# Kernel tuning notes

Hardware: AMD Instinct MI355X
Metric: run time of the kernel (lower is better)

Reference implementation:

```python
import jax, jax.numpy as jnp
import numpy as np

ATOM_FDIM = 35
BOND_FDIM = 5
MAX_NB = 10
HIDDEN = 128
DEPTH = 6
N_ATOMS = 100000
N_BONDS = 220000
N_MESS = 20000
N_MOLS = 2000


def setup_inputs() -> dict:
    key = jax.random.key(0)
    ks = jax.random.split(key, 10)
    fatoms = jax.random.uniform(ks[0], (N_ATOMS, ATOM_FDIM), dtype=jnp.float32)
    fbonds = jax.random.uniform(ks[1], (N_BONDS, ATOM_FDIM + BOND_FDIM), dtype=jnp.float32)
    tree_message = jax.random.normal(ks[2], (N_MESS, HIDDEN), dtype=jnp.float32)
    tree_message = tree_message.at[0].set(0.0)  # index 0 is the zero-padding message
    agraph = jax.random.randint(ks[3], (N_ATOMS, MAX_NB), 0, N_MESS + N_BONDS, dtype=jnp.int32)
    bgraph = jax.random.randint(ks[4], (N_BONDS, MAX_NB), 0, N_MESS + N_BONDS, dtype=jnp.int32)
    mol_ids = jnp.sort(jax.random.randint(ks[5], (N_ATOMS,), 0, N_MOLS, dtype=jnp.int32))
    # learned parameters (torch Linear stores W as [out, in]; we keep [in, out])
    def lin(k, fan_in, fan_out):
        bound = 1.0 / np.sqrt(fan_in)
        return jax.random.uniform(k, (fan_in, fan_out), minval=-bound, maxval=bound, dtype=jnp.float32)
    W_i = lin(ks[6], ATOM_FDIM + BOND_FDIM, HIDDEN)
    W_h = lin(ks[7], HIDDEN, HIDDEN)
    W_o = lin(ks[8], ATOM_FDIM + HIDDEN, HIDDEN)
    b_o = jax.random.uniform(ks[9], (HIDDEN,), minval=-1.0 / np.sqrt(ATOM_FDIM + HIDDEN), maxval=1.0 / np.sqrt(ATOM_FDIM + HIDDEN), dtype=jnp.float32)
    return {
        'fatoms': fatoms, 'fbonds': fbonds, 'tree_message': tree_message,
        'agraph': agraph, 'bgraph': bgraph, 'mol_ids': mol_ids, 'n_mols': N_MOLS,
        'W_i': W_i, 'W_h': W_h, 'W_o': W_o, 'b_o': b_o,
    }


def reference(fatoms, fbonds, tree_message, agraph, bgraph, mol_ids, n_mols, W_i, W_h, W_o, b_o):
    binput = fbonds @ W_i                    # [B, H]
    graph_message = jax.nn.relu(binput)
    for _ in range(DEPTH - 1):
        message = jnp.concatenate([tree_message, graph_message], axis=0)  # [M+B, H]
        nei = message[bgraph].sum(axis=1)    # gather [B, MAX_NB, H] -> sum -> [B, H]
        graph_message = jax.nn.relu(binput + nei @ W_h)
    message = jnp.concatenate([tree_message, graph_message], axis=0)
    nei_a = message[agraph].sum(axis=1)      # [A, H]
    ainput = jnp.concatenate([fatoms, nei_a], axis=1)  # [A, ATOM_FDIM+H]
    atom_hiddens = jax.nn.relu(ainput @ W_o + b_o)     # [A, H]
    # mean-pool per molecule (scope)
    sums = jax.ops.segment_sum(atom_hiddens, mol_ids, num_segments=n_mols)
    counts = jax.ops.segment_sum(jnp.ones((atom_hiddens.shape[0],), dtype=atom_hiddens.dtype), mol_ids, num_segments=n_mols)
    mol_vecs = sums / jnp.maximum(counts, 1.0)[:, None]
    return mol_vecs
```

## Files before the change

### kernel.cpp

```cpp
#include <hip/hip_runtime.h>

#define N_ATOMS   100000
#define N_BONDS   220000
#define N_MESS    20000
#define N_MSG     (N_MESS + N_BONDS)
#define ATOM_FDIM 35
#define BOND_FDIM 5
#define BOND_IN   (ATOM_FDIM + BOND_FDIM)
#define H         128
#define MAX_NB    10
#define DEPTH     6
#define KO        (ATOM_FDIM + H)
#define KC        192

typedef __attribute__((ext_vector_type(8))) short short8;
typedef __attribute__((ext_vector_type(4))) float f32x4;

static __device__ __forceinline__ unsigned short f2bf(float f) {
    union { float f; unsigned int i; } v; v.f = f;
    unsigned int x = v.i;
    return (unsigned short)((x + 0x7FFFu + ((x >> 16) & 1u)) >> 16);
}

static __device__ __forceinline__ float ub2f(unsigned int v, int b) {
    return (float)((v >> (b * 8)) & 0xffu);
}

static __device__ __forceinline__ unsigned char q8(float x) {
    int q = __float2int_rn(x);
    q = q < 0 ? 0 : (q > 255 ? 255 : q);
    return (unsigned char)q;
}

#define PTa (N_BONDS * BOND_IN)
#define PTb (PTa + H * KC)
#define PTc (PTb + H * KC)

__global__ __launch_bounds__(256) void prep(
    const float* __restrict__ fbonds,
    const float* __restrict__ Wi, const float* __restrict__ Wh,
    const float* __restrict__ Wo,
    ushort* __restrict__ fbc, ushort* __restrict__ WT,
    ushort* __restrict__ WoT, float* __restrict__ out, int n_out)
{
    int i = blockIdx.x * 256 + threadIdx.x;
    if (i < PTa) {
        fbc[i] = f2bf(fbonds[i]);
    } else if (i < PTb) {
        int j = i - PTa;
        int n = j / KC, k = j - n * KC;
        float v = (k < BOND_IN) ? Wi[k * H + n]
                : (k < BOND_IN + H) ? Wh[(k - BOND_IN) * H + n] : 0.f;
        WT[j] = f2bf(v);
    } else if (i < PTc) {
        int j = i - PTb;
        int n = j / KC, k = j - n * KC;
        float v = (k < H) ? Wo[(ATOM_FDIM + k) * H + n]
                : (k < KO) ? Wo[(k - H) * H + n] : 0.f;
        WoT[j] = f2bf(v);
    } else {
        int j = i - PTc;
        if (j < n_out) out[j] = 0.f;
    }
}

__global__ __launch_bounds__(256) void qtree(
    const float* __restrict__ tree,
    unsigned char* __restrict__ qA, unsigned char* __restrict__ qB,
    float2* __restrict__ sA, float2* __restrict__ sB)
{
    int row = blockIdx.x * 4 + (threadIdx.x >> 6);
    int lane = threadIdx.x & 63;
    float2 v = *(const float2*)&tree[(size_t)row * H + lane * 2];
    float mx = fmaxf(v.x, v.y), mn = fminf(v.x, v.y);
    #pragma unroll
    for (int d = 1; d <= 32; d <<= 1) {
        mx = fmaxf(mx, __shfl_xor(mx, d));
        mn = fminf(mn, __shfl_xor(mn, d));
    }
    float rng = mx - mn;
    float inv = (rng > 0.f) ? 255.f / rng : 0.f;
    int q0 = q8((v.x - mn) * inv);
    int q1 = q8((v.y - mn) * inv);
    unsigned short pk = (unsigned short)(q0 | (q1 << 8));
    ((unsigned short*)qA)[(size_t)row * 64 + lane] = pk;
    ((unsigned short*)qB)[(size_t)row * 64 + lane] = pk;
    if (lane == 0) {
        float2 s = make_float2(rng * (1.f / 255.f), mn);
        sA[row] = s; sB[row] = s;
    }
}

static __device__ __forceinline__ uint4 gather8(
    const unsigned char* __restrict__ msgq, const float2* __restrict__ scl,
    const int* __restrict__ gidx, int c16)
{
    int idx[MAX_NB];
    #pragma unroll
    for (int n = 0; n < MAX_NB; n++) idx[n] = gidx[n];
    float2 so[MAX_NB];
    uint2 d[MAX_NB];
    #pragma unroll
    for (int n = 0; n < MAX_NB; n++) {
        so[n] = scl[idx[n]];
        d[n] = *(const uint2*)(msgq + (size_t)idx[n] * H + c16 * 8);
    }
    float s0=0.f,s1=0.f,s2=0.f,s3=0.f,s4=0.f,s5=0.f,s6=0.f,s7=0.f;
    float off = 0.f;
    #pragma unroll
    for (int n = 0; n < MAX_NB; n++) {
        float sc = so[n].x; off += so[n].y;
        s0 += sc * ub2f(d[n].x, 0); s1 += sc * ub2f(d[n].x, 1);
        s2 += sc * ub2f(d[n].x, 2); s3 += sc * ub2f(d[n].x, 3);
        s4 += sc * ub2f(d[n].y, 0); s5 += sc * ub2f(d[n].y, 1);
        s6 += sc * ub2f(d[n].y, 2); s7 += sc * ub2f(d[n].y, 3);
    }
    s0 += off; s1 += off; s2 += off; s3 += off;
    s4 += off; s5 += off; s6 += off; s7 += off;
    uint4 pk;
    pk.x = ((unsigned)f2bf(s1) << 16) | (unsigned)f2bf(s0);
    pk.y = ((unsigned)f2bf(s3) << 16) | (unsigned)f2bf(s2);
    pk.z = ((unsigned)f2bf(s5) << 16) | (unsigned)f2bf(s4);
    pk.w = ((unsigned)f2bf(s7) << 16) | (unsigned)f2bf(s6);
    return pk;
}

static __device__ __forceinline__ void quant_epilogue(
    f32x4 c00, f32x4 c01, f32x4 c10, f32x4 c11,
    int tid, int row_base,
    float* rmx, float* qp,
    unsigned char* __restrict__ gq, float2* __restrict__ scout)
{
    int lane = tid & 63, wv = tid >> 6;
    int m_lane = lane & 15, quad = lane >> 4;
    int n0 = wv * 32;

    float v00[4], v01[4], v10[4], v11[4];
    #pragma unroll
    for (int r = 0; r < 4; r++) {
        v00[r] = fmaxf(c00[r], 0.f); v01[r] = fmaxf(c01[r], 0.f);
        v10[r] = fmaxf(c10[r], 0.f); v11[r] = fmaxf(c11[r], 0.f);
    }
    #pragma unroll
    for (int r = 0; r < 4; r++) {
        float mx0 = fmaxf(v00[r], v01[r]);
        float mx1 = fmaxf(v10[r], v11[r]);
        #pragma unroll
        for (int d = 1; d <= 8; d <<= 1) {
            mx0 = fmaxf(mx0, __shfl_xor(mx0, d));
            mx1 = fmaxf(mx1, __shfl_xor(mx1, d));
        }
        if (m_lane == 0) {
            rmx[(quad * 4 + r) * 4 + wv]      = mx0;
            rmx[(quad * 4 + r + 16) * 4 + wv] = mx1;
        }
    }
    __syncthreads();
    if (tid < 32) {
        float mx = fmaxf(fmaxf(rmx[tid * 4], rmx[tid * 4 + 1]),
                         fmaxf(rmx[tid * 4 + 2], rmx[tid * 4 + 3]));
        qp[tid] = (mx > 0.f) ? 255.f / mx : 0.f;
        scout[row_base + tid] = make_float2(mx * (1.f / 255.f), 0.f);
    }
    __syncthreads();
    #pragma unroll
    for (int r = 0; r < 4; r++) {
        int r0 = quad * 4 + r, r1 = r0 + 16;
        float i0 = qp[r0], i1 = qp[r1];
        gq[(size_t)(row_base + r0) * H + n0 + m_lane]      = q8(v00[r] * i0);
        gq[(size_t)(row_base + r0) * H + n0 + 16 + m_lane] = q8(v01[r] * i0);
        gq[(size_t)(row_base + r1) * H + n0 + m_lane]      = q8(v10[r] * i1);
        gq[(size_t)(row_base + r1) * H + n0 + 16 + m_lane] = q8(v11[r] * i1);
    }
}

__global__ __launch_bounds__(256, 4) void binput0(
    const ushort* __restrict__ fbc, const ushort* __restrict__ WT,
    unsigned char* __restrict__ gq_out, float2* __restrict__ sc_out)
{
    __shared__ ushort Xlds[32 * 25 * 8];
    __shared__ float rmx[32 * 4];
    __shared__ float qp[32];

    int tid = threadIdx.x;
    int bond0 = blockIdx.x * 32;
    int lane = tid & 63, wv = tid >> 6;

    if (tid < 160) {
        int b = tid / 5, k8 = tid - b * 5;
        *(short8*)&Xlds[(b * 25 + k8) * 8] =
            *(const short8*)&fbc[(size_t)bond0 * BOND_IN + tid * 8];
    }
    if (tid < 96) {
        int b = tid / 3, k8 = 5 + (tid - b * 3);
        *(float4*)&Xlds[(b * 25 + k8) * 8] = float4{0.f, 0.f, 0.f, 0.f};
    }
    __syncthreads();

    int n0 = wv * 32;
    int m_lane = lane & 15, quad = lane >> 4;
    f32x4 c00 = {0,0,0,0}, c01 = {0,0,0,0}, c10 = {0,0,0,0}, c11 = {0,0,0,0};

    #pragma unroll
    for (int s = 0; s < 2; s++) {
        short8 a0 = *(const short8*)&Xlds[((m_lane)      * 25 + s * 4 + quad) * 8];
        short8 a1 = *(const short8*)&Xlds[((16 + m_lane) * 25 + s * 4 + quad) * 8];
        short8 b0 = *(const short8*)&WT[(size_t)(n0 + m_lane)      * KC + s * 32 + quad * 8];
        short8 b1 = *(const short8*)&WT[(size_t)(n0 + 16 + m_lane) * KC + s * 32 + quad * 8];
        c00 = __builtin_amdgcn_mfma_f32_16x16x32_bf16(a0, b0, c00, 0, 0, 0);
        c01 = __builtin_amdgcn_mfma_f32_16x16x32_bf16(a0, b1, c01, 0, 0, 0);
        c10 = __builtin_amdgcn_mfma_f32_16x16x32_bf16(a1, b0, c10, 0, 0, 0);
        c11 = __builtin_amdgcn_mfma_f32_16x16x32_bf16(a1, b1, c11, 0, 0, 0);
    }

    quant_epilogue(c00, c01, c10, c11, tid, bond0, rmx, qp, gq_out, sc_out);
}

__global__ __launch_bounds__(256, 4) void mp_round(
    const unsigned char* __restrict__ msg_in, const float2* __restrict__ sc_in,
    const ushort* __restrict__ fbc, const int* __restrict__ bgraph,
    const ushort* __restrict__ WT,
    unsigned char* __restrict__ gq_out, float2* __restrict__ sc_out)
{
    __shared__ ushort Xlds[32 * 25 * 8];
    __shared__ float rmx[32 * 4];
    __shared__ float qp[32];

    int tid = threadIdx.x;
    int bond0 = blockIdx.x * 32;
    int lane = tid & 63, wv = tid >> 6;
    int q = lane >> 4, c16 = lane & 15;

    if (tid < 160) {
        int b = tid / 5, k8 = tid - b * 5;
        *(short8*)&Xlds[(b * 25 + k8) * 8] =
            *(const short8*)&fbc[(size_t)bond0 * BOND_IN + tid * 8];
    }
    if (tid < 96) {
        int b = tid / 3, k8 = 21 + (tid - b * 3);
        *(float4*)&Xlds[(b * 25 + k8) * 8] = float4{0.f, 0.f, 0.f, 0.f};
    }
    #pragma unroll
    for (int g = 0; g < 2; g++) {
        int b = wv + 4 * (g * 4 + q);
        uint4 pk = gather8(msg_in, sc_in, bgraph + (size_t)(bond0 + b) * MAX_NB, c16);
        *(uint4*)&Xlds[(b * 25 + 5 + c16) * 8] = pk;
    }
    __syncthreads();

    int n0 = wv * 32;
    int m_lane = lane & 15, quad = lane >> 4;
    f32x4 c00 = {0,0,0,0}, c01 = {0,0,0,0}, c10 = {0,0,0,0}, c11 = {0,0,0,0};

    #pragma unroll
    for (int s = 0; s < KC / 32; s++) {
        short8 a0 = *(const short8*)&Xlds[((m_lane)      * 25 + s * 4 + quad) * 8];
        short8 a1 = *(const short8*)&Xlds[((16 + m_lane) * 25 + s * 4 + quad) * 8];
        short8 b0 = *(const short8*)&WT[(size_t)(n0 + m_lane)      * KC + s * 32 + quad * 8];
        short8 b1 = *(const short8*)&WT[(size_t)(n0 + 16 + m_lane) * KC + s * 32 + quad * 8];
        c00 = __builtin_amdgcn_mfma_f32_16x16x32_bf16(a0, b0, c00, 0, 0, 0);
        c01 = __builtin_amdgcn_mfma_f32_16x16x32_bf16(a0, b1, c01, 0, 0, 0);
        c10 = __builtin_amdgcn_mfma_f32_16x16x32_bf16(a1, b0, c10, 0, 0, 0);
        c11 = __builtin_amdgcn_mfma_f32_16x16x32_bf16(a1, b1, c11, 0, 0, 0);
    }

    quant_epilogue(c00, c01, c10, c11, tid, bond0, rmx, qp, gq_out, sc_out);
}

__global__ __launch_bounds__(256, 4) void atom_mfma(
    const float* __restrict__ fatoms, const unsigned char* __restrict__ msg,
    const float2* __restrict__ scl,
    const int* __restrict__ agraph, const ushort* __restrict__ WoT,
    const float* __restrict__ bo, const int* __restrict__ mol_ids,
    float* __restrict__ out)
{
    __shared__ ushort Xlds[32 * 25 * 8];
    __shared__ float htile[32 * H];
    __shared__ int mlds[32];

    int tid = threadIdx.x;
    int a0 = blockIdx.x * 32;
    int lane = tid & 63, wv = tid >> 6;
    int q = lane >> 4, c16 = lane & 15;

    for (int i = tid; i < 32 * ATOM_FDIM; i += 256) {
        int b = i / ATOM_FDIM, t = i - b * ATOM_FDIM;
        int k = H + t;
        Xlds[(b * 25 + (k >> 3)) * 8 + (k & 7)] = f2bf(fatoms[(size_t)a0 * ATOM_FDIM + i]);
    }
    if (tid < 160) {
        int b = tid / 5, k = 163 + (tid - b * 5);
        Xlds[(b * 25 + (k >> 3)) * 8 + (k & 7)] = 0;
    }
    if (tid < 96) {
        int b = tid / 3, k8 = 21 + (tid - b * 3);
        *(float4*)&Xlds[(b * 25 + k8) * 8] = float4{0.f, 0.f, 0.f, 0.f};
    }
    if (tid < 32) mlds[tid] = mol_ids[a0 + tid];
    #pragma unroll
    for (int g = 0; g < 2; g++) {
        int b = wv + 4 * (g * 4 + q);
        uint4 pk = gather8(msg, scl, agraph + (size_t)(a0 + b) * MAX_NB, c16);
        *(uint4*)&Xlds[(b * 25 + c16) * 8] = pk;
    }
    __syncthreads();

    int n0 = wv * 32;
    int m_lane = lane & 15, quad = lane >> 4;
    float bias0 = bo[n0 + m_lane], bias1 = bo[n0 + 16 + m_lane];
    f32x4 c00 = {bias0, bias0, bias0, bias0};
    f32x4 c01 = {bias1, bias1, bias1, bias1};
    f32x4 c10 = {bias0, bias0, bias0, bias0};
    f32x4 c11 = {bias1, bias1, bias1, bias1};

    #pragma unroll
    for (int s = 0; s < KC / 32; s++) {
        short8 a0f = *(const short8*)&Xlds[((m_lane)      * 25 + s * 4 + quad) * 8];
        short8 a1f = *(const short8*)&Xlds[((16 + m_lane) * 25 + s * 4 + quad) * 8];
        short8 b0f = *(const short8*)&WoT[(size_t)(n0 + m_lane)      * KC + s * 32 + quad * 8];
        short8 b1f = *(const short8*)&WoT[(size_t)(n0 + 16 + m_lane) * KC + s * 32 + quad * 8];
        c00 = __builtin_amdgcn_mfma_f32_16x16x32_bf16(a0f, b0f, c00, 0, 0, 0);
        c01 = __builtin_amdgcn_mfma_f32_16x16x32_bf16(a0f, b1f, c01, 0, 0, 0);
        c10 = __builtin_amdgcn_mfma_f32_16x16x32_bf16(a1f, b0f, c10, 0, 0, 0);
        c11 = __builtin_amdgcn_mfma_f32_16x16x32_bf16(a1f, b1f, c11, 0, 0, 0);
    }

    #pragma unroll
    for (int r = 0; r < 4; r++) {
        int r0 = quad * 4 + r, r1 = r0 + 16;
        htile[r0 * H + n0 + m_lane]      = fmaxf(c00[r], 0.f);
        htile[r0 * H + n0 + 16 + m_lane] = fmaxf(c01[r], 0.f);
        htile[r1 * H + n0 + m_lane]      = fmaxf(c10[r], 0.f);
        htile[r1 * H + n0 + 16 + m_lane] = fmaxf(c11[r], 0.f);
    }
    __syncthreads();

    if (tid < H) {
        int j = tid;
        float acc = 0.f;
        int cur = mlds[0];
        for (int r = 0; r < 32; r++) {
            int m = mlds[r];
            if (m != cur) {
                atomicAdd(&out[(size_t)cur * H + j], acc);
                acc = 0.f; cur = m;
            }
            acc += htile[r * H + j];
        }
        atomicAdd(&out[(size_t)cur * H + j], acc);
    }
}

__global__ __launch_bounds__(128) void pool_div(
    const int* __restrict__ mol_ids, float* __restrict__ out, int n_atoms)
{
    int m = blockIdx.x;
    int j = threadIdx.x;

    int lo = 0, hi = n_atoms;
    while (lo < hi) { int mid = (lo + hi) >> 1; if (mol_ids[mid] < m) lo = mid + 1; else hi = mid; }
    int start = lo;
    hi = n_atoms;
    while (lo < hi) { int mid = (lo + hi) >> 1; if (mol_ids[mid] < m + 1) lo = mid + 1; else hi = mid; }
    int end = lo;

    out[(size_t)m * H + j] /= fmaxf((float)(end - start), 1.f);
}

extern "C" void kernel_launch(void* const* d_in, const int* in_sizes, int n_in,
                              void* d_out, int out_size, void* d_ws, size_t ws_size,
                              hipStream_t stream)
{
    const float* fatoms  = (const float*)d_in[0];
    const float* fbonds  = (const float*)d_in[1];
    const float* tree    = (const float*)d_in[2];
    const int*   agraph  = (const int*)d_in[3];
    const int*   bgraph  = (const int*)d_in[4];
    const int*   mol_ids = (const int*)d_in[5];
    const float* W_i = (const float*)d_in[7];
    const float* W_h = (const float*)d_in[8];
    const float* W_o = (const float*)d_in[9];
    const float* b_o = (const float*)d_in[10];
    float* out = (float*)d_out;

    unsigned char* mqA = (unsigned char*)d_ws;
    unsigned char* mqB = mqA + (size_t)N_MSG * H;
    float2* scA = (float2*)(mqB + (size_t)N_MSG * H);
    float2* scB = scA + N_MSG;
    ushort* WT  = (ushort*)(scB + N_MSG);
    ushort* WoT = WT + (size_t)H * KC;
    ushort* fbc = WoT + (size_t)H * KC;

    int prep_total = PTc + out_size;
    prep<<<(prep_total + 255) / 256, 256, 0, stream>>>(
        fbonds, W_i, W_h, W_o, fbc, WT, WoT, out, out_size);

    qtree<<<N_MESS / 4, 256, 0, stream>>>(tree, mqA, mqB, scA, scB);

    binput0<<<N_BONDS / 32, 256, 0, stream>>>(fbc, WT,
        mqA + (size_t)N_MESS * H, scA + N_MESS);

    const unsigned char* tin = mqA; const float2* sin = scA;
    unsigned char* tout = mqB; float2* sout = scB;
    for (int r = 0; r < DEPTH - 1; r++) {
        mp_round<<<N_BONDS / 32, 256, 0, stream>>>(tin, sin, fbc, bgraph, WT,
            tout + (size_t)N_MESS * H, sout + N_MESS);
        const unsigned char* t1 = tin; tin = tout; tout = (unsigned char*)t1;
        const float2* t2 = sin; sin = sout; sout = (float2*)t2;
    }

    atom_mfma<<<N_ATOMS / 32, 256, 0, stream>>>(fatoms, tin, sin, agraph, WoT, b_o,
                                                mol_ids, out);

    int n_mols = out_size / H;
    pool_div<<<n_mols, 128, 0, stream>>>(mol_ids, out, N_ATOMS);
}
```

Before: 626.6 us.

## Pack messages as 7-bit values with per-group exponent scales inline

Replaces the per-row uint8 message plus separate float2 scale/offset with 7-bit signed values packed eight per uint2, storing a shared power-of-two scale code in the spare top bits. Each neighbor gather then needs only one 8-byte load instead of an extra scale lookup, and the quantization epilogue no longer needs a block-wide row max reduction with two barriers. Neighbor index tables are repacked to a stride of 12 so they can be read with vector loads. Precision drops to 7 bits with coarser power-of-two scaling, and the prep kernel does extra index copying.

Measured after the change: 543.4 us. -13.3%, faster.

```diff
diff --git a/kernel.cpp b/kernel.cpp
--- a/kernel.cpp
+++ b/kernel.cpp
@@ -9,12 +9,18 @@
 #define BOND_IN   (ATOM_FDIM + BOND_FDIM)
 #define H         128
 #define MAX_NB    10
+#define NB_PAD    12
 #define DEPTH     6
 #define KO        (ATOM_FDIM + H)
 #define KC        192
+#define SC_BIAS   887u
 
 typedef __attribute__((ext_vector_type(8))) short short8;
 typedef __attribute__((ext_vector_type(4))) float f32x4;
+
+static __device__ __forceinline__ float asf(unsigned int u) {
+    union { unsigned int i; float f; } v; v.i = u; return v.f;
+}
 
 static __device__ __forceinline__ unsigned short f2bf(float f) {
     union { float f; unsigned int i; } v; v.f = f;
@@ -22,26 +28,30 @@
     return (unsigned short)((x + 0x7FFFu + ((x >> 16) & 1u)) >> 16);
 }
 
-static __device__ __forceinline__ float ub2f(unsigned int v, int b) {
-    return (float)((v >> (b * 8)) & 0xffu);
-}
-
-static __device__ __forceinline__ unsigned char q8(float x) {
-    int q = __float2int_rn(x);
-    q = q < 0 ? 0 : (q > 255 ? 255 : q);
-    return (unsigned char)q;
+static __device__ __forceinline__ int bfe7(unsigned int w, int p) {
+    return ((int)(w << (25 - p))) >> 25;
+}
+
+static __device__ __forceinline__ unsigned int pack7(unsigned int d) {
+    return (d & 0x7Fu) | ((d >> 8) & 0x7Fu) << 7 |
+           ((d >> 16) & 0x7Fu) << 14 | ((d >> 24) & 0x7Fu) << 21;
 }
 
 #define PTa (N_BONDS * BOND_IN)
 #define PTb (PTa + H * KC)
 #define PTc (PTb + H * KC)
+#define PTd (PTc + N_BONDS * MAX_NB)
+#define PTe (PTd + N_ATOMS * MAX_NB)
 
 __global__ __launch_bounds__(256) void prep(
     const float* __restrict__ fbonds,
     const float* __restrict__ Wi, const float* __restrict__ Wh,
     const float* __restrict__ Wo,
+    const int* __restrict__ bgraph, const int* __restrict__ agraph,
     ushort* __restrict__ fbc, ushort* __restrict__ WT,
-    ushort* __restrict__ WoT, float* __restrict__ out, int n_out)
+    ushort* __restrict__ WoT,
+    int* __restrict__ bgP, int* __restrict__ agP,
+    float* __restrict__ out, int n_out)
 {
     int i = blockIdx.x * 256 + threadIdx.x;
     if (i < PTa) {
@@ -58,65 +68,77 @@
         float v = (k < H) ? Wo[(ATOM_FDIM + k) * H + n]
                 : (k < KO) ? Wo[(k - H) * H + n] : 0.f;
         WoT[j] = f2bf(v);
+    } else if (i < PTd) {
+        int j = i - PTc;
+        int b = j / MAX_NB, n = j - b * MAX_NB;
+        bgP[b * NB_PAD + n] = bgraph[j];
+    } else if (i < PTe) {
+        int j = i - PTd;
+        int a = j / MAX_NB, n = j - a * MAX_NB;
+        agP[a * NB_PAD + n] = agraph[j];
     } else {
-        int j = i - PTc;
+        int j = i - PTe;
         if (j < n_out) out[j] = 0.f;
     }
 }
 
 __global__ __launch_bounds__(256) void qtree(
     const float* __restrict__ tree,
-    unsigned char* __restrict__ qA, unsigned char* __restrict__ qB,
-    float2* __restrict__ sA, float2* __restrict__ sB)
-{
-    int row = blockIdx.x * 4 + (threadIdx.x >> 6);
-    int lane = threadIdx.x & 63;
-    float2 v = *(const float2*)&tree[(size_t)row * H + lane * 2];
-    float mx = fmaxf(v.x, v.y), mn = fminf(v.x, v.y);
-    #pragma unroll
-    for (int d = 1; d <= 32; d <<= 1) {
-        mx = fmaxf(mx, __shfl_xor(mx, d));
-        mn = fminf(mn, __shfl_xor(mn, d));
-    }
-    float rng = mx - mn;
-    float inv = (rng > 0.f) ? 255.f / rng : 0.f;
-    int q0 = q8((v.x - mn) * inv);
-    int q1 = q8((v.y - mn) * inv);
-    unsigned short pk = (unsigned short)(q0 | (q1 << 8));
-    ((unsigned short*)qA)[(size_t)row * 64 + lane] = pk;
-    ((unsigned short*)qB)[(size_t)row * 64 + lane] = pk;
-    if (lane == 0) {
-        float2 s = make_float2(rng * (1.f / 255.f), mn);
-        sA[row] = s; sB[row] = s;
-    }
-}
-
-static __device__ __forceinline__ uint4 gather8(
-    const unsigned char* __restrict__ msgq, const float2* __restrict__ scl,
-    const int* __restrict__ gidx, int c16)
-{
-    int idx[MAX_NB];
-    #pragma unroll
-    for (int n = 0; n < MAX_NB; n++) idx[n] = gidx[n];
-    float2 so[MAX_NB];
+    uint2* __restrict__ qA, uint2* __restrict__ qB)
+{
+    int t = blockIdx.x * 256 + threadIdx.x;
+    int row = t >> 4, L = t & 15;
+    float4 a = *(const float4*)&tree[(size_t)row * H + L * 8];
+    float4 b = *(const float4*)&tree[(size_t)row * H + L * 8 + 4];
+    float m8 = fmaxf(fmaxf(fmaxf(fabsf(a.x), fabsf(a.y)), fmaxf(fabsf(a.z), fabsf(a.w))),
+                     fmaxf(fmaxf(fabsf(b.x), fabsf(b.y)), fmaxf(fabsf(b.z), fabsf(b.w))));
+    float t_ = m8 * (1.f / 63.f);
+    int code = (int)((__float_as_uint(t_) + 0xFFFFFu) >> 20) - (int)SC_BIAS;
+    code = code < 1 ? 1 : (code > 255 ? 255 : code);
+    float inv = __builtin_amdgcn_rcpf(asf(((unsigned)code + SC_BIAS) << 20));
+    int q[8];
+    float v[8] = {a.x, a.y, a.z, a.w, b.x, b.y, b.z, b.w};
+    #pragma unroll
+    for (int k = 0; k < 8; k++) {
+        int qq = __float2int_rn(v[k] * inv);
+        q[k] = qq < -63 ? -63 : (qq > 63 ? 63 : qq);
+    }
+    unsigned lo = (q[0] & 0x7F) | (q[1] & 0x7F) << 7 | (q[2] & 0x7F) << 14 |
+                  (q[3] & 0x7F) << 21 | ((unsigned)code & 0xF) << 28;
+    unsigned hi = (q[4] & 0x7F) | (q[5] & 0x7F) << 7 | (q[6] & 0x7F) << 14 |
+                  (q[7] & 0x7F) << 21 | ((unsigned)code >> 4) << 28;
+    uint2 pk = {lo, hi};
+    qA[t] = pk; qB[t] = pk;
+}
+
+static __device__ __forceinline__ uint4 gather7(
+    const uint2* __restrict__ msgq, const int* __restrict__ gidx, int c16)
+{
+    uint4 i0 = *(const uint4*)gidx;
+    uint4 i1 = *(const uint4*)(gidx + 4);
+    uint2 i2 = *(const uint2*)(gidx + 8);
+    int idx[MAX_NB] = {(int)i0.x, (int)i0.y, (int)i0.z, (int)i0.w,
+                       (int)i1.x, (int)i1.y, (int)i1.z, (int)i1.w,
+                       (int)i2.x, (int)i2.y};
     uint2 d[MAX_NB];
     #pragma unroll
+    for (int n = 0; n < MAX_NB; n++)
+        d[n] = msgq[(size_t)idx[n] * 16 + c16];
+    float s0=0.f,s1=0.f,s2=0.f,s3=0.f,s4=0.f,s5=0.f,s6=0.f,s7=0.f;
+    #pragma unroll
     for (int n = 0; n < MAX_NB; n++) {
-        so[n] = scl[idx[n]];
-        d[n] = *(const uint2*)(msgq + (size_t)idx[n] * H + c16 * 8);
-    }
-    float s0=0.f,s1=0.f,s2=0.f,s3=0.f,s4=0.f,s5=0.f,s6=0.f,s7=0.f;
-    float off = 0.f;
-    #pragma unroll
-    for (int n = 0; n < MAX_NB; n++) {
-        float sc = so[n].x; off += so[n].y;
-        s0 += sc * ub2f(d[n].x, 0); s1 += sc * ub2f(d[n].x, 1);
-        s2 += sc * ub2f(d[n].x, 2); s3 += sc * ub2f(d[n].x, 3);
-        s4 += sc * ub2f(d[n].y, 0); s5 += sc * ub2f(d[n].y, 1);
-        s6 += sc * ub2f(d[n].y, 2); s7 += sc * ub2f(d[n].y, 3);
-    }
-    s0 += off; s1 += off; s2 += off; s3 += off;
-    s4 += off; s5 += off; s6 += off; s7 += off;
+        unsigned lo = d[n].x, hi = d[n].y;
+        unsigned code = (lo >> 28) | ((hi >> 28) << 4);
+        float scf = asf((code + SC_BIAS) << 20);
+        s0 += scf * (float)bfe7(lo, 0);
+        s1 += scf * (float)bfe7(lo, 7);
+        s2 += scf * (float)bfe7(lo, 14);
+        s3 += scf * (float)bfe7(lo, 21);
+        s4 += scf * (float)bfe7(hi, 0);
+        s5 += scf * (float)bfe7(hi, 7);
+        s6 += scf * (float)bfe7(hi, 14);
+        s7 += scf * (float)bfe7(hi, 21);
+    }
     uint4 pk;
     pk.x = ((unsigned)f2bf(s1) << 16) | (unsigned)f2bf(s0);
     pk.y = ((unsigned)f2bf(s3) << 16) | (unsigned)f2bf(s2);
@@ -125,62 +147,62 @@
     return pk;
 }
 
-static __device__ __forceinline__ void quant_epilogue(
+static __device__ __forceinline__ void quant_epilogue7(
     f32x4 c00, f32x4 c01, f32x4 c10, f32x4 c11,
     int tid, int row_base,
-    float* rmx, float* qp,
-    unsigned char* __restrict__ gq, float2* __restrict__ scout)
+    unsigned int* qlds_u32 , unsigned char* clds ,
+    uint2* __restrict__ gq)
 {
     int lane = tid & 63, wv = tid >> 6;
     int m_lane = lane & 15, quad = lane >> 4;
     int n0 = wv * 32;
-
-    float v00[4], v01[4], v10[4], v11[4];
-    #pragma unroll
-    for (int r = 0; r < 4; r++) {
-        v00[r] = fmaxf(c00[r], 0.f); v01[r] = fmaxf(c01[r], 0.f);
-        v10[r] = fmaxf(c10[r], 0.f); v11[r] = fmaxf(c11[r], 0.f);
-    }
-    #pragma unroll
-    for (int r = 0; r < 4; r++) {
-        float mx0 = fmaxf(v00[r], v01[r]);
-        float mx1 = fmaxf(v10[r], v11[r]);
+    char* qlds = (char*)qlds_u32;
+
+    #pragma unroll
+    for (int st = 0; st < 4; st++) {
         #pragma unroll
-        for (int d = 1; d <= 8; d <<= 1) {
-            mx0 = fmaxf(mx0, __shfl_xor(mx0, d));
-            mx1 = fmaxf(mx1, __shfl_xor(mx1, d));
+        for (int r = 0; r < 4; r++) {
+            float x = (st == 0) ? c00[r] : (st == 1) ? c01[r] : (st == 2) ? c10[r] : c11[r];
+            x = fmaxf(x, 0.f);
+            float mx = x;
+            mx = fmaxf(mx, __shfl_xor(mx, 1));
+            mx = fmaxf(mx, __shfl_xor(mx, 2));
+            mx = fmaxf(mx, __shfl_xor(mx, 4));
+            float t_ = mx * (1.f / 63.f);
+            int code = (int)((__float_as_uint(t_) + 0xFFFFFu) >> 20) - (int)SC_BIAS;
+            code = code < 1 ? 1 : (code > 255 ? 255 : code);
+            float inv = __builtin_amdgcn_rcpf(asf(((unsigned)code + SC_BIAS) << 20));
+            int q = __float2int_rn(x * inv);
+            q = q > 63 ? 63 : q;
+            int row = quad * 4 + r + ((st & 2) ? 16 : 0);
+            int col = n0 + m_lane + ((st & 1) ? 16 : 0);
+            qlds[row * 128 + col] = (char)q;
+            if ((m_lane & 7) == 0) clds[row * 16 + (col >> 3)] = (unsigned char)code;
         }
-        if (m_lane == 0) {
-            rmx[(quad * 4 + r) * 4 + wv]      = mx0;
-            rmx[(quad * 4 + r + 16) * 4 + wv] = mx1;
-        }
     }
     __syncthreads();
-    if (tid < 32) {
-        float mx = fmaxf(fmaxf(rmx[tid * 4], rmx[tid * 4 + 1]),
-                         fmaxf(rmx[tid * 4 + 2], rmx[tid * 4 + 3]));
-        qp[tid] = (mx > 0.f) ? 255.f / mx : 0.f;
-        scout[row_base + tid] = make_float2(mx * (1.f / 255.f), 0.f);
-    }
-    __syncthreads();
-    #pragma unroll
-    for (int r = 0; r < 4; r++) {
-        int r0 = quad * 4 + r, r1 = r0 + 16;
-        float i0 = qp[r0], i1 = qp[r1];
-        gq[(size_t)(row_base + r0) * H + n0 + m_lane]      = q8(v00[r] * i0);
-        gq[(size_t)(row_base + r0) * H + n0 + 16 + m_lane] = q8(v01[r] * i0);
-        gq[(size_t)(row_base + r1) * H + n0 + m_lane]      = q8(v10[r] * i1);
-        gq[(size_t)(row_base + r1) * H + n0 + 16 + m_lane] = q8(v11[r] * i1);
+    {
+        int s = tid * 2;
+        int row = s >> 4, grp = s & 15;
+        uint4 w = *(const uint4*)(qlds + row * 128 + grp * 8);
+        unsigned code0 = clds[row * 16 + grp];
+        unsigned code1 = clds[row * 16 + grp + 1];
+        uint4 o;
+        o.x = pack7(w.x) | (code0 & 0xFu) << 28;
+        o.y = pack7(w.y) | (code0 >> 4) << 28;
+        o.z = pack7(w.z) | (code1 & 0xFu) << 28;
+        o.w = pack7(w.w) | (code1 >> 4) << 28;
+        *(uint4*)&gq[(size_t)(row_base + row) * 16 + grp] = o;
     }
 }
 
 __global__ __launch_bounds__(256, 4) void binput0(
     const ushort* __restrict__ fbc, const ushort* __restrict__ WT,
-    unsigned char* __restrict__ gq_out, float2* __restrict__ sc_out)
+    uint2* __restrict__ gq_out)
 {
     __shared__ ushort Xlds[32 * 25 * 8];
-    __shared__ float rmx[32 * 4];
-    __shared__ float qp[32];
+    __shared__ __align__(16) unsigned int qlds[32 * 32];
+    __shared__ unsigned char clds[32 * 16];
 
     int tid = threadIdx.x;
     int bond0 = blockIdx.x * 32;
@@ -213,18 +235,18 @@
         c11 = __builtin_amdgcn_mfma_f32_16x16x32_bf16(a1, b1, c11, 0, 0, 0);
     }
 
-    quant_epilogue(c00, c01, c10, c11, tid, bond0, rmx, qp, gq_out, sc_out);
+    quant_epilogue7(c00, c01, c10, c11, tid, bond0, qlds, clds, gq_out);
 }
 
 __global__ __launch_bounds__(256, 4) void mp_round(
-    const unsigned char* __restrict__ msg_in, const float2* __restrict__ sc_in,
-    const ushort* __restrict__ fbc, const int* __restrict__ bgraph,
+    const uint2* __restrict__ msg_in,
+    const ushort* __restrict__ fbc, const int* __restrict__ bgraphP,
     const ushort* __restrict__ WT,
-    unsigned char* __restrict__ gq_out, float2* __restrict__ sc_out)
+    uint2* __restrict__ gq_out)
 {
     __shared__ ushort Xlds[32 * 25 * 8];
-    __shared__ float rmx[32 * 4];
-    __shared__ float qp[32];
+    __shared__ __align__(16) unsigned int qlds[32 * 32];
+    __shared__ unsigned char clds[32 * 16];
 
     int tid = threadIdx.x;
     int bond0 = blockIdx.x * 32;
@@ -243,7 +265,7 @@
     #pragma unroll
     for (int g = 0; g < 2; g++) {
         int b = wv + 4 * (g * 4 + q);
-        uint4 pk = gather8(msg_in, sc_in, bgraph + (size_t)(bond0 + b) * MAX_NB, c16);
+        uint4 pk = gather7(msg_in, bgraphP + (size_t)(bond0 + b) * NB_PAD, c16);
         *(uint4*)&Xlds[(b * 25 + 5 + c16) * 8] = pk;
     }
     __syncthreads();
@@ -264,13 +286,12 @@
         c11 = __builtin_amdgcn_mfma_f32_16x16x32_bf16(a1, b1, c11, 0, 0, 0);
     }
 
-    quant_epilogue(c00, c01, c10, c11, tid, bond0, rmx, qp, gq_out, sc_out);
+    quant_epilogue7(c00, c01, c10, c11, tid, bond0, qlds, clds, gq_out);
 }
 
 __global__ __launch_bounds__(256, 4) void atom_mfma(
-    const float* __restrict__ fatoms, const unsigned char* __restrict__ msg,
-    const float2* __restrict__ scl,
-    const int* __restrict__ agraph, const ushort* __restrict__ WoT,
+    const float* __restrict__ fatoms, const uint2* __restrict__ msg,
+    const int* __restrict__ agraphP, const ushort* __restrict__ WoT,
     const float* __restrict__ bo, const int* __restrict__ mol_ids,
     float* __restrict__ out)
 {
@@ -300,7 +321,7 @@
     #pragma unroll
     for (int g = 0; g < 2; g++) {
         int b = wv + 4 * (g * 4 + q);
-        uint4 pk = gather8(msg, scl, agraph + (size_t)(a0 + b) * MAX_NB, c16);
+        uint4 pk = gather7(msg, agraphP + (size_t)(a0 + b) * NB_PAD, c16);
         *(uint4*)&Xlds[(b * 25 + c16) * 8] = pk;
     }
     __syncthreads();
@@ -383,33 +404,31 @@
     const float* b_o = (const float*)d_in[10];
     float* out = (float*)d_out;
 
-    unsigned char* mqA = (unsigned char*)d_ws;
-    unsigned char* mqB = mqA + (size_t)N_MSG * H;
-    float2* scA = (float2*)(mqB + (size_t)N_MSG * H);
-    float2* scB = scA + N_MSG;
-    ushort* WT  = (ushort*)(scB + N_MSG);
+    uint2* mqA = (uint2*)d_ws;
+    uint2* mqB = mqA + (size_t)N_MSG * 16;
+    ushort* WT  = (ushort*)(mqB + (size_t)N_MSG * 16);
     ushort* WoT = WT + (size_t)H * KC;
     ushort* fbc = WoT + (size_t)H * KC;
-
-    int prep_total = PTc + out_size;
+    int* bgP = (int*)(fbc + (size_t)N_BONDS * BOND_IN);
+    int* agP = bgP + (size_t)N_BONDS * NB_PAD;
+
+    int prep_total = PTe + out_size;
     prep<<<(prep_total + 255) / 256, 256, 0, stream>>>(
-        fbonds, W_i, W_h, W_o, fbc, WT, WoT, out, out_size);
-
-    qtree<<<N_MESS / 4, 256, 0, stream>>>(tree, mqA, mqB, scA, scB);
-
-    binput0<<<N_BONDS / 32, 256, 0, stream>>>(fbc, WT,
-        mqA + (size_t)N_MESS * H, scA + N_MESS);
-
-    const unsigned char* tin = mqA; const float2* sin = scA;
-    unsigned char* tout = mqB; float2* sout = scB;
+        fbonds, W_i, W_h, W_o, bgraph, agraph, fbc, WT, WoT, bgP, agP, out, out_size);
+
+    qtree<<<(N_MESS * 16) / 256, 256, 0, stream>>>(tree, mqA, mqB);
+
+    binput0<<<N_BONDS / 32, 256, 0, stream>>>(fbc, WT, mqA + (size_t)N_MESS * 16);
+
+    const uint2* tin = mqA;
+    uint2* tout = mqB;
     for (int r = 0; r < DEPTH - 1; r++) {
-        mp_round<<<N_BONDS / 32, 256, 0, stream>>>(tin, sin, fbc, bgraph, WT,
-            tout + (size_t)N_MESS * H, sout + N_MESS);
-        const unsigned char* t1 = tin; tin = tout; tout = (unsigned char*)t1;
-        const float2* t2 = sin; sin = sout; sout = (float2*)t2;
-    }
-
-    atom_mfma<<<N_ATOMS / 32, 256, 0, stream>>>(fatoms, tin, sin, agraph, WoT, b_o,
+        mp_round<<<N_BONDS / 32, 256, 0, stream>>>(tin, fbc, bgP, WT,
+                                                   tout + (size_t)N_MESS * 16);
+        const uint2* t1 = tin; tin = tout; tout = (uint2*)t1;
+    }
+
+    atom_mfma<<<N_ATOMS / 32, 256, 0, stream>>>(fatoms, tin, agP, WoT, b_o,
                                                 mol_ids, out);
 
     int n_mols = out_size / H;
```

## Pad neighbor indices, stage quantized output in LDS, use packed bf16 convert

Applied to the files above, without the earlier changes.

The prep kernel now copies bgraph and agraph into 12-wide padded index arrays, so each gather can read its indices with vector loads. The quantization epilogue writes u8 values into a shared-memory tile and then stores each row as coalesced 16-byte chunks instead of scattered byte stores. The gather also uses the v_cvt_pk_bf16_f32 instruction instead of manual rounding. The costs are an extra prep pass over the index arrays, more workspace, an extra LDS buffer and an extra barrier per block.

Result: faster. 597.6 us (-4.6%).

```diff
diff --git a/kernel.cpp b/kernel.cpp
--- a/kernel.cpp
+++ b/kernel.cpp
@@ -9,9 +9,11 @@
 #define BOND_IN   (ATOM_FDIM + BOND_FDIM)
 #define H         128
 #define MAX_NB    10
+#define NB_PAD    12
 #define DEPTH     6
 #define KO        (ATOM_FDIM + H)
 #define KC        192
+#define QLDS_STR  144
 
 typedef __attribute__((ext_vector_type(8))) short short8;
 typedef __attribute__((ext_vector_type(4))) float f32x4;
@@ -26,22 +28,27 @@
     return (float)((v >> (b * 8)) & 0xffu);
 }
 
-static __device__ __forceinline__ unsigned char q8(float x) {
+static __device__ __forceinline__ unsigned int q8c(float x) {
     int q = __float2int_rn(x);
     q = q < 0 ? 0 : (q > 255 ? 255 : q);
-    return (unsigned char)q;
+    return (unsigned int)q;
 }
 
 #define PTa (N_BONDS * BOND_IN)
 #define PTb (PTa + H * KC)
 #define PTc (PTb + H * KC)
+#define PTd (PTc + N_BONDS * MAX_NB)
+#define PTe (PTd + N_ATOMS * MAX_NB)
 
 __global__ __launch_bounds__(256) void prep(
     const float* __restrict__ fbonds,
     const float* __restrict__ Wi, const float* __restrict__ Wh,
     const float* __restrict__ Wo,
+    const int* __restrict__ bgraph, const int* __restrict__ agraph,
     ushort* __restrict__ fbc, ushort* __restrict__ WT,
-    ushort* __restrict__ WoT, float* __restrict__ out, int n_out)
+    ushort* __restrict__ WoT,
+    int* __restrict__ bgP, int* __restrict__ agP,
+    float* __restrict__ out, int n_out)
 {
     int i = blockIdx.x * 256 + threadIdx.x;
     if (i < PTa) {
@@ -58,15 +65,23 @@
         float v = (k < H) ? Wo[(ATOM_FDIM + k) * H + n]
                 : (k < KO) ? Wo[(k - H) * H + n] : 0.f;
         WoT[j] = f2bf(v);
+    } else if (i < PTd) {
+        int j = i - PTc;
+        int b = j / MAX_NB, n = j - b * MAX_NB;
+        bgP[b * NB_PAD + n] = bgraph[j];
+    } else if (i < PTe) {
+        int j = i - PTd;
+        int a = j / MAX_NB, n = j - a * MAX_NB;
+        agP[a * NB_PAD + n] = agraph[j];
     } else {
-        int j = i - PTc;
+        int j = i - PTe;
         if (j < n_out) out[j] = 0.f;
     }
 }
 
 __global__ __launch_bounds__(256) void qtree(
     const float* __restrict__ tree,
-    unsigned char* __restrict__ qA, unsigned char* __restrict__ qB,
+    ushort* __restrict__ qA, ushort* __restrict__ qB,
     float2* __restrict__ sA, float2* __restrict__ sB)
 {
     int row = blockIdx.x * 4 + (threadIdx.x >> 6);
@@ -80,30 +95,33 @@
     }
     float rng = mx - mn;
     float inv = (rng > 0.f) ? 255.f / rng : 0.f;
-    int q0 = q8((v.x - mn) * inv);
-    int q1 = q8((v.y - mn) * inv);
+    unsigned q0 = q8c((v.x - mn) * inv);
+    unsigned q1 = q8c((v.y - mn) * inv);
     unsigned short pk = (unsigned short)(q0 | (q1 << 8));
-    ((unsigned short*)qA)[(size_t)row * 64 + lane] = pk;
-    ((unsigned short*)qB)[(size_t)row * 64 + lane] = pk;
+    qA[(size_t)row * 64 + lane] = pk;
+    qB[(size_t)row * 64 + lane] = pk;
     if (lane == 0) {
         float2 s = make_float2(rng * (1.f / 255.f), mn);
         sA[row] = s; sB[row] = s;
     }
 }
 
-static __device__ __forceinline__ uint4 gather8(
-    const unsigned char* __restrict__ msgq, const float2* __restrict__ scl,
+static __device__ __forceinline__ uint4 gather_u8(
+    const uint2* __restrict__ msgq, const float2* __restrict__ scl,
     const int* __restrict__ gidx, int c16)
 {
-    int idx[MAX_NB];
-    #pragma unroll
-    for (int n = 0; n < MAX_NB; n++) idx[n] = gidx[n];
+    uint4 i0 = *(const uint4*)gidx;
+    uint4 i1 = *(const uint4*)(gidx + 4);
+    uint2 i2 = *(const uint2*)(gidx + 8);
+    int idx[MAX_NB] = {(int)i0.x, (int)i0.y, (int)i0.z, (int)i0.w,
+                       (int)i1.x, (int)i1.y, (int)i1.z, (int)i1.w,
+                       (int)i2.x, (int)i2.y};
     float2 so[MAX_NB];
     uint2 d[MAX_NB];
     #pragma unroll
     for (int n = 0; n < MAX_NB; n++) {
         so[n] = scl[idx[n]];
-        d[n] = *(const uint2*)(msgq + (size_t)idx[n] * H + c16 * 8);
+        d[n] = msgq[(size_t)idx[n] * 16 + c16];
     }
     float s0=0.f,s1=0.f,s2=0.f,s3=0.f,s4=0.f,s5=0.f,s6=0.f,s7=0.f;
     float off = 0.f;
@@ -118,18 +136,18 @@
     s0 += off; s1 += off; s2 += off; s3 += off;
     s4 += off; s5 += off; s6 += off; s7 += off;
     uint4 pk;
-    pk.x = ((unsigned)f2bf(s1) << 16) | (unsigned)f2bf(s0);
-    pk.y = ((unsigned)f2bf(s3) << 16) | (unsigned)f2bf(s2);
-    pk.z = ((unsigned)f2bf(s5) << 16) | (unsigned)f2bf(s4);
-    pk.w = ((unsigned)f2bf(s7) << 16) | (unsigned)f2bf(s6);
+    asm("v_cvt_pk_bf16_f32 %0, %1, %2" : "=v"(pk.x) : "v"(s0), "v"(s1));
+    asm("v_cvt_pk_bf16_f32 %0, %1, %2" : "=v"(pk.y) : "v"(s2), "v"(s3));
+    asm("v_cvt_pk_bf16_f32 %0, %1, %2" : "=v"(pk.z) : "v"(s4), "v"(s5));
+    asm("v_cvt_pk_bf16_f32 %0, %1, %2" : "=v"(pk.w) : "v"(s6), "v"(s7));
     return pk;
 }
 
-static __device__ __forceinline__ void quant_epilogue(
+static __device__ __forceinline__ void u8_epilogue(
     f32x4 c00, f32x4 c01, f32x4 c10, f32x4 c11,
     int tid, int row_base,
-    float* rmx, float* qp,
-    unsigned char* __restrict__ gq, float2* __restrict__ scout)
+    float* rmx , float* qp , char* qlds,
+    uint4* __restrict__ gq4, float2* __restrict__ scout)
 {
     int lane = tid & 63, wv = tid >> 6;
     int m_lane = lane & 15, quad = lane >> 4;
@@ -167,18 +185,23 @@
     for (int r = 0; r < 4; r++) {
         int r0 = quad * 4 + r, r1 = r0 + 16;
         float i0 = qp[r0], i1 = qp[r1];
-        gq[(size_t)(row_base + r0) * H + n0 + m_lane]      = q8(v00[r] * i0);
-        gq[(size_t)(row_base + r0) * H + n0 + 16 + m_lane] = q8(v01[r] * i0);
-        gq[(size_t)(row_base + r1) * H + n0 + m_lane]      = q8(v10[r] * i1);
-        gq[(size_t)(row_base + r1) * H + n0 + 16 + m_lane] = q8(v11[r] * i1);
-    }
+        qlds[r0 * QLDS_STR + n0 + m_lane]      = (char)q8c(v00[r] * i0);
+        qlds[r0 * QLDS_STR + n0 + 16 + m_lane] = (char)q8c(v01[r] * i0);
+        qlds[r1 * QLDS_STR + n0 + m_lane]      = (char)q8c(v10[r] * i1);
+        qlds[r1 * QLDS_STR + n0 + 16 + m_lane] = (char)q8c(v11[r] * i1);
+    }
+    __syncthreads();
+    int row = tid >> 3, seg = tid & 7;
+    uint4 w = *(const uint4*)(qlds + row * QLDS_STR + seg * 16);
+    gq4[(size_t)(row_base + row) * 8 + seg] = w;
 }
 
 __global__ __launch_bounds__(256, 4) void binput0(
     const ushort* __restrict__ fbc, const ushort* __restrict__ WT,
-    unsigned char* __restrict__ gq_out, float2* __restrict__ sc_out)
+    uint4* __restrict__ gq_out, float2* __restrict__ sc_out)
 {
     __shared__ ushort Xlds[32 * 25 * 8];
+    __shared__ __align__(16) char qlds[32 * QLDS_STR];
     __shared__ float rmx[32 * 4];
     __shared__ float qp[32];
 
@@ -213,16 +236,17 @@
         c11 = __builtin_amdgcn_mfma_f32_16x16x32_bf16(a1, b1, c11, 0, 0, 0);
     }
 
-    quant_epilogue(c00, c01, c10, c11, tid, bond0, rmx, qp, gq_out, sc_out);
+    u8_epilogue(c00, c01, c10, c11, tid, bond0, rmx, qp, qlds, gq_out, sc_out);
 }
 
 __global__ __launch_bounds__(256, 4) void mp_round(
-    const unsigned char* __restrict__ msg_in, const float2* __restrict__ sc_in,
-    const ushort* __restrict__ fbc, const int* __restrict__ bgraph,
+    const uint2* __restrict__ msg_in, const float2* __restrict__ sc_in,
+    const ushort* __restrict__ fbc, const int* __restrict__ bgraphP,
     const ushort* __restrict__ WT,
-    unsigned char* __restrict__ gq_out, float2* __restrict__ sc_out)
+    uint4* __restrict__ gq_out, float2* __restrict__ sc_out)
 {
     __shared__ ushort Xlds[32 * 25 * 8];
+    __shared__ __align__(16) char qlds[32 * QLDS_STR];
     __shared__ float rmx[32 * 4];
     __shared__ float qp[32];
 
@@ -243,7 +267,8 @@
     #pragma unroll
     for (int g = 0; g < 2; g++) {
         int b = wv + 4 * (g * 4 + q);
-        uint4 pk = gather8(msg_in, sc_in, bgraph + (size_t)(bond0 + b) * MAX_NB, c16);
+        uint4 pk = gather_u8(msg_in, sc_in,
+                             bgraphP + (size_t)(bond0 + b) * NB_PAD, c16);
         *(uint4*)&Xlds[(b * 25 + 5 + c16) * 8] = pk;
     }
     __syncthreads();
@@ -264,13 +289,13 @@
         c11 = __builtin_amdgcn_mfma_f32_16x16x32_bf16(a1, b1, c11, 0, 0, 0);
     }
 
-    quant_epilogue(c00, c01, c10, c11, tid, bond0, rmx, qp, gq_out, sc_out);
+    u8_epilogue(c00, c01, c10, c11, tid, bond0, rmx, qp, qlds, gq_out, sc_out);
 }
 
 __global__ __launch_bounds__(256, 4) void atom_mfma(
-    const float* __restrict__ fatoms, const unsigned char* __restrict__ msg,
+    const float* __restrict__ fatoms, const uint2* __restrict__ msg,
     const float2* __restrict__ scl,
-    const int* __restrict__ agraph, const ushort* __restrict__ WoT,
+    const int* __restrict__ agraphP, const ushort* __restrict__ WoT,
     const float* __restrict__ bo, const int* __restrict__ mol_ids,
     float* __restrict__ out)
 {
@@ -300,7 +325,8 @@
     #pragma unroll
     for (int g = 0; g < 2; g++) {
         int b = wv + 4 * (g * 4 + q);
-        uint4 pk = gather8(msg, scl, agraph + (size_t)(a0 + b) * MAX_NB, c16);
+        uint4 pk = gather_u8(msg, scl,
+                             agraphP + (size_t)(a0 + b) * NB_PAD, c16);
         *(uint4*)&Xlds[(b * 25 + c16) * 8] = pk;
     }
     __syncthreads();
@@ -383,33 +409,35 @@
     const float* b_o = (const float*)d_in[10];
     float* out = (float*)d_out;
 
-    unsigned char* mqA = (unsigned char*)d_ws;
-    unsigned char* mqB = mqA + (size_t)N_MSG * H;
-    float2* scA = (float2*)(mqB + (size_t)N_MSG * H);
+    uint2* mqA = (uint2*)d_ws;
+    uint2* mqB = mqA + (size_t)N_MSG * 16;
+    float2* scA = (float2*)(mqB + (size_t)N_MSG * 16);
     float2* scB = scA + N_MSG;
     ushort* WT  = (ushort*)(scB + N_MSG);
     ushort* WoT = WT + (size_t)H * KC;
     ushort* fbc = WoT + (size_t)H * KC;
-
-    int prep_total = PTc + out_size;
+    int* bgP = (int*)(fbc + (size_t)N_BONDS * BOND_IN);
+    int* agP = bgP + (size_t)N_BONDS * NB_PAD;
+
+    int prep_total = PTe + out_size;
     prep<<<(prep_total + 255) / 256, 256, 0, stream>>>(
-        fbonds, W_i, W_h, W_o, fbc, WT, WoT, out, out_size);
-
-    qtree<<<N_MESS / 4, 256, 0, stream>>>(tree, mqA, mqB, scA, scB);
+        fbonds, W_i, W_h, W_o, bgraph, agraph, fbc, WT, WoT, bgP, agP, out, out_size);
+
+    qtree<<<N_MESS / 4, 256, 0, stream>>>(tree, (ushort*)mqA, (ushort*)mqB, scA, scB);
 
     binput0<<<N_BONDS / 32, 256, 0, stream>>>(fbc, WT,
-        mqA + (size_t)N_MESS * H, scA + N_MESS);
-
-    const unsigned char* tin = mqA; const float2* sin = scA;
-    unsigned char* tout = mqB; float2* sout = scB;
+        (uint4*)(mqA + (size_t)N_MESS * 16), scA + N_MESS);
+
+    const uint2* tin = mqA; const float2* sin = scA;
+    uint2* tout = mqB; float2* sout = scB;
     for (int r = 0; r < DEPTH - 1; r++) {
-        mp_round<<<N_BONDS / 32, 256, 0, stream>>>(tin, sin, fbc, bgraph, WT,
-            tout + (size_t)N_MESS * H, sout + N_MESS);
-        const unsigned char* t1 = tin; tin = tout; tout = (unsigned char*)t1;
+        mp_round<<<N_BONDS / 32, 256, 0, stream>>>(tin, sin, fbc, bgP, WT,
+            (uint4*)(tout + (size_t)N_MESS * 16), sout + N_MESS);
+        const uint2* t1 = tin; tin = tout; tout = (uint2*)t1;
         const float2* t2 = sin; sin = sout; sout = (float2*)t2;
     }
 
-    atom_mfma<<<N_ATOMS / 32, 256, 0, stream>>>(fatoms, tin, sin, agraph, WoT, b_o,
+    atom_mfma<<<N_ATOMS / 32, 256, 0, stream>>>(fatoms, tin, sin, agP, WoT, b_o,
                                                 mol_ids, out);
 
     int n_mols = out_size / H;
```
